# Optimization experiments

Hardware: AMD Instinct MI355X
Metric: run time of the kernel (lower is better)

## Reference

```python
import jax, jax.numpy as jnp
import numpy as np

B, L, E = 128, 512, 128
NUM_Q, NUM_C, DIFF = 10000, 300, 100


def _lin(k, fan_in, fan_out):
    kw, kb = jax.random.split(k)
    s = 1.0 / np.sqrt(fan_in)
    W = jax.random.uniform(kw, (fan_in, fan_out), jnp.float32, -s, s)
    b = jax.random.uniform(kb, (fan_out,), jnp.float32, -s, s)
    return W, b


def setup_inputs() -> dict:
    key = jax.random.key(0)
    ks = jax.random.split(key, 24)
    inp = {
        "q": jax.random.randint(ks[0], (B, L), 0, NUM_Q),
        "c": jax.random.randint(ks[1], (B, L), 0, NUM_C),
        "sd": jax.random.randint(ks[2], (B, L), 0, DIFF + 99),
        "qd": jax.random.randint(ks[3], (B, L), 0, DIFF + 99),
        "a": jax.random.randint(ks[4], (B, L), 0, 2 * NUM_Q + 1),
        "qshft": jax.random.randint(ks[5], (B, L), 0, NUM_Q),
        "cshft": jax.random.randint(ks[6], (B, L), 0, NUM_C),
        "sdshft": jax.random.randint(ks[7], (B, L), 0, DIFF + 99),
        "qdshft": jax.random.randint(ks[8], (B, L), 0, DIFF + 99),
        "knowledge": jax.random.normal(ks[9], (1, E), jnp.float32) * 0.1,
        "q_tab": jax.random.normal(ks[10], (NUM_Q + 1, E), jnp.float32),
        "c_tab": jax.random.normal(ks[11], (NUM_C + 1, E), jnp.float32),
        "sd_tab": jax.random.normal(ks[12], (DIFF + 100, E), jnp.float32),
        "qd_tab": jax.random.normal(ks[13], (DIFF + 100, E), jnp.float32),
        "a_tab": jax.random.normal(ks[14], (2 * NUM_Q + 2, E), jnp.float32),
    }
    for name, fan_in, ki in [("1", 4 * E, 15), ("2", E, 16), ("3", E, 17),
                             ("4", 2 * E, 18), ("5", 2 * E, 19), ("6", 4 * E, 20)]:
        W, b = _lin(ks[ki], fan_in, E)
        inp[f"W{name}"], inp[f"b{name}"] = W, b
    Wf, bf = _lin(ks[21], E, 10)
    inp["Wf"], inp["bf"] = Wf, bf
    return inp


def reference(q, c, sd, qd, a, qshft, cshft, sdshft, qdshft,
              knowledge, q_tab, c_tab, sd_tab, qd_tab, a_tab,
              W1, b1, W2, b2, W3, b3, W4, b4, W5, b5, W6, b6, Wf, bf):
    # Embedding lookups  [B, L, E]
    q_e, c_e = q_tab[q], c_tab[c]
    sd_e, qd_e = sd_tab[sd], qd_tab[qd]
    a_e = a_tab[a]
    # input_data = linear_1(cat(q,c,sd,qd))  [B, L, E]
    inp = jnp.concatenate([q_e, c_e, sd_e, qd_e], -1) @ W1 + b1
    # (target_data in the torch code is dead: never used for the output)

    k0 = jnp.broadcast_to(knowledge, (q.shape[0], knowledge.shape[1]))  # [B, E]

    def step(k, xs):
        x, sd1, a1, qd1 = xs  # each [B, E]
        qq = x - k
        SDFt = jax.nn.sigmoid(qq @ W2 + b2) * jnp.tanh(qq @ W3 + b3)  # dropout=eval
        xa = jnp.concatenate([SDFt, a1], -1)
        PKAt = jax.nn.sigmoid(xa @ W4 + b4) * jnp.tanh(xa @ W5 + b5)
        ins = jnp.concatenate([k, a1, sd1, qd1], -1)
        gK = jax.nn.sigmoid(ins @ W6 + b6)
        k_new = gK * k + (1.0 - gK) * PKAt
        return k_new, k_new @ Wf + bf

    xs = (jnp.swapaxes(inp, 0, 1), jnp.swapaxes(sd_e, 0, 1),
          jnp.swapaxes(a_e, 0, 1), jnp.swapaxes(qd_e, 0, 1))  # [L, B, E]
    _, logits = jax.lax.scan(step, k0, xs)  # [L, B, 10]
    return jax.nn.sigmoid(jnp.swapaxes(logits, 0, 1))  # [B, L, 10]
```

## Files before the change

kernel.cpp:

```cpp
#include <hip/hip_runtime.h>
#include <hip/hip_bf16.h>
#include <stdint.h>

#define E_DIM 128
#define L_SEQ 512
#define B_SZ  128

typedef _Float16 h2 __attribute__((ext_vector_type(2)));
typedef _Float16 f16x8 __attribute__((ext_vector_type(8)));
typedef float f32x4 __attribute__((ext_vector_type(4)));

constexpr size_t SZ_W12  = 512 * 128 * 4;
constexpr size_t SZ_TQ   = (size_t)10001 * 128 * 2 * 4;
constexpr size_t SZ_TC   = (size_t)301 * 128 * 2 * 4;
constexpr size_t SZ_TSD  = (size_t)200 * 128 * 4 * 4;
constexpr size_t SZ_TQD  = (size_t)200 * 128 * 4 * 4;
constexpr size_t SZ_TA45 = (size_t)20002 * 128 * 2 * 4;
constexpr size_t SZ_TA6  = (size_t)20002 * 128 * 4;
constexpr size_t SZ_K    = (size_t)B_SZ * L_SEQ * 128 * 4;

constexpr size_t OFF_W12  = 0;
constexpr size_t OFF_W13  = OFF_W12 + SZ_W12;
constexpr size_t OFF_BV2  = OFF_W13 + SZ_W12;
constexpr size_t OFF_BV3  = OFF_BV2 + 512;
constexpr size_t OFF_TQ   = OFF_BV3 + 512;
constexpr size_t OFF_TC   = OFF_TQ + SZ_TQ;
constexpr size_t OFF_TSD  = OFF_TC + SZ_TC;
constexpr size_t OFF_TQD  = OFF_TSD + SZ_TSD;
constexpr size_t OFF_TA45 = OFF_TQD + SZ_TQD;
constexpr size_t OFF_TA6  = OFF_TA45 + SZ_TA45;
constexpr size_t OFF_K    = OFF_TA6 + SZ_TA6;

__device__ __forceinline__ float fdot2f(unsigned int a, unsigned int b, float c) {
#if __has_builtin(__builtin_amdgcn_fdot2)
  return __builtin_amdgcn_fdot2(__builtin_bit_cast(h2, a), __builtin_bit_cast(h2, b), c, false);
#else
  h2 x = __builtin_bit_cast(h2, a), y = __builtin_bit_cast(h2, b);
  return c + (float)x[0] * (float)y[0] + (float)x[1] * (float)y[1];
#endif
}

__device__ __forceinline__ unsigned int packh2(float a, float b) {
  h2 v; v[0] = (_Float16)a; v[1] = (_Float16)b;
  return __builtin_bit_cast(unsigned int, v);
}

__device__ __forceinline__ float fsig(float x) {
  float t = __builtin_amdgcn_exp2f(-1.4426950408889634f * x);
  return __builtin_amdgcn_rcpf(1.0f + t);
}
__device__ __forceinline__ float ftanh(float x) {
  float t = __builtin_amdgcn_exp2f(2.8853900817779268f * x);
  return 1.0f - 2.0f * __builtin_amdgcn_rcpf(t + 1.0f);
}

#define BARRIER_RAW() asm volatile("s_waitcnt lgkmcnt(0)\n\ts_barrier" ::: "memory")

__global__ __launch_bounds__(256, 2) void prepA_kernel(
    const float* __restrict__ W1, const float* __restrict__ W2, const float* __restrict__ W3,
    const float* __restrict__ b1, const float* __restrict__ b2, const float* __restrict__ b3,
    char* __restrict__ ws) {
  float* W12 = (float*)(ws + OFF_W12);
  float* W13 = (float*)(ws + OFF_W13);
  float* bv2 = (float*)(ws + OFF_BV2);
  float* bv3 = (float*)(ws + OFF_BV3);
  const int blk = blockIdx.x, tid = threadIdx.x;
  if (blk < 512) {
    const int m = blk >> 8;
    const int rp = blk & 255;
    const float* M = m ? W3 : W2;
    float* dst = m ? W13 : W12;
    const int rr = tid >> 7, j = tid & 127;
    const int r = rp * 2 + rr;
    __shared__ float rowL[2][128];
    rowL[rr][j] = W1[r * 128 + j];
    __syncthreads();
    float acc = 0.0f;
#pragma unroll 8
    for (int t = 0; t < 128; t++) acc += rowL[rr][t] * M[t * 128 + j];
    dst[r * 128 + j] = acc;
  } else if (tid < 128) {
    float a2 = b2[tid], a3 = b3[tid];
    for (int t = 0; t < 128; t++) {
      float bb = b1[t];
      a2 += bb * W2[t * 128 + tid];
      a3 += bb * W3[t * 128 + tid];
    }
    bv2[tid] = a2;
    bv3[tid] = a3;
  }
}

__global__ __launch_bounds__(256, 2) void gemm_tab1_kernel(
    const float* __restrict__ q_tab, const float* __restrict__ c_tab,
    const float* __restrict__ sd_tab, const float* __restrict__ qd_tab,
    const float* __restrict__ a_tab,
    const float* __restrict__ W4, const float* __restrict__ W5, const float* __restrict__ W6,
    const float* __restrict__ b4, const float* __restrict__ b5, const float* __restrict__ b6,
    char* __restrict__ ws) {
  __shared__ _Float16 BT[128][136];
  __shared__ _Float16 At[32][136];
  __shared__ float biasL[128];

  const float* W12 = (const float*)(ws + OFF_W12);
  const float* W13 = (const float*)(ws + OFF_W13);
  const float* bv2f = (const float*)(ws + OFF_BV2);
  const float* bv3f = (const float*)(ws + OFF_BV3);

  const int bid = blockIdx.x, tid = threadIdx.x;
  const int wv = tid >> 6, ln = tid & 63;

  int task, rb;
  if      (bid < 79)  { task = 0;  rb = bid; }
  else if (bid < 158) { task = 1;  rb = bid - 79; }
  else if (bid < 161) { task = 2;  rb = bid - 158; }
  else if (bid < 164) { task = 3;  rb = bid - 161; }
  else if (bid < 166) { task = 4;  rb = bid - 164; }
  else if (bid < 168) { task = 5;  rb = bid - 166; }
  else if (bid < 170) { task = 6;  rb = bid - 168; }
  else if (bid < 172) { task = 7;  rb = bid - 170; }
  else if (bid < 174) { task = 8;  rb = bid - 172; }
  else if (bid < 176) { task = 9;  rb = bid - 174; }
  else if (bid < 333) { task = 10; rb = bid - 176; }
  else if (bid < 490) { task = 11; rb = bid - 333; }
  else                { task = 12; rb = bid - 490; }

  const float* src; int rows; const float* Bsrc; const float* bias;
  float* dst; int STR, ILV, SLOT;
  switch (task) {
    case 0:  src = q_tab;  rows = 10001; Bsrc = W12;           bias = bv2f;    dst = (float*)(ws + OFF_TQ);   STR = 256; ILV = 2; SLOT = 0; break;
    case 1:  src = q_tab;  rows = 10001; Bsrc = W13;           bias = bv3f;    dst = (float*)(ws + OFF_TQ);   STR = 256; ILV = 2; SLOT = 1; break;
    case 2:  src = c_tab;  rows = 301;   Bsrc = W12 + 128*128; bias = nullptr; dst = (float*)(ws + OFF_TC);   STR = 256; ILV = 2; SLOT = 0; break;
    case 3:  src = c_tab;  rows = 301;   Bsrc = W13 + 128*128; bias = nullptr; dst = (float*)(ws + OFF_TC);   STR = 256; ILV = 2; SLOT = 1; break;
    case 4:  src = sd_tab; rows = 200;   Bsrc = W12 + 256*128; bias = nullptr; dst = (float*)(ws + OFF_TSD);  STR = 512; ILV = 4; SLOT = 0; break;
    case 5:  src = sd_tab; rows = 200;   Bsrc = W13 + 256*128; bias = nullptr; dst = (float*)(ws + OFF_TSD);  STR = 512; ILV = 4; SLOT = 1; break;
    case 6:  src = sd_tab; rows = 200;   Bsrc = W6  + 256*128; bias = nullptr; dst = (float*)(ws + OFF_TSD);  STR = 512; ILV = 4; SLOT = 2; break;
    case 7:  src = qd_tab; rows = 200;   Bsrc = W12 + 384*128; bias = nullptr; dst = (float*)(ws + OFF_TQD);  STR = 512; ILV = 4; SLOT = 0; break;
    case 8:  src = qd_tab; rows = 200;   Bsrc = W13 + 384*128; bias = nullptr; dst = (float*)(ws + OFF_TQD);  STR = 512; ILV = 4; SLOT = 1; break;
    case 9:  src = qd_tab; rows = 200;   Bsrc = W6  + 384*128; bias = nullptr; dst = (float*)(ws + OFF_TQD);  STR = 512; ILV = 4; SLOT = 2; break;
    case 10: src = a_tab;  rows = 20002; Bsrc = W4  + 128*128; bias = b4;      dst = (float*)(ws + OFF_TA45); STR = 256; ILV = 2; SLOT = 0; break;
    case 11: src = a_tab;  rows = 20002; Bsrc = W5  + 128*128; bias = b5;      dst = (float*)(ws + OFF_TA45); STR = 256; ILV = 2; SLOT = 1; break;
    default: src = a_tab;  rows = 20002; Bsrc = W6  + 128*128; bias = b6;      dst = (float*)(ws + OFF_TA6);  STR = 128; ILV = 1; SLOT = 0; break;
  }

#pragma unroll
  for (int r = 0; r < 8; r++) {
    const int k = (tid >> 4) + r * 16;
    const int j0 = (tid & 15) * 8;
    float4 v0 = *(const float4*)(Bsrc + k * 128 + j0);
    float4 v1 = *(const float4*)(Bsrc + k * 128 + j0 + 4);
    BT[j0 + 0][k] = (_Float16)v0.x; BT[j0 + 1][k] = (_Float16)v0.y;
    BT[j0 + 2][k] = (_Float16)v0.z; BT[j0 + 3][k] = (_Float16)v0.w;
    BT[j0 + 4][k] = (_Float16)v1.x; BT[j0 + 5][k] = (_Float16)v1.y;
    BT[j0 + 6][k] = (_Float16)v1.z; BT[j0 + 7][k] = (_Float16)v1.w;
  }
  if (tid < 128) biasL[tid] = bias ? bias[tid] : 0.0f;
  __syncthreads();

  f16x8 bfr[2][4];
#pragma unroll
  for (int ct = 0; ct < 2; ct++)
#pragma unroll
    for (int kt = 0; kt < 4; kt++) {
      const int col = wv * 32 + ct * 16 + (ln & 15);
      const int k = kt * 32 + (ln >> 4) * 8;
      bfr[ct][kt] = *(const f16x8*)&BT[col][k];
    }
  float bvl[2] = { biasL[wv * 32 + (ln & 15)], biasL[wv * 32 + 16 + (ln & 15)] };

  const int row_base = rb * 128;
  for (int ch = 0; ch < 4; ch++) {
    const int row0 = row_base + ch * 32;
    {
      const int r = tid >> 3, cb = (tid & 7) * 16;
      int sr = row0 + r; if (sr >= rows) sr = rows - 1;
      const float4* s4 = (const float4*)(src + (size_t)sr * 128 + cb);
      float4 v0 = s4[0], v1 = s4[1], v2 = s4[2], v3 = s4[3];
      f16x8 lo, hi;
      lo[0] = (_Float16)v0.x; lo[1] = (_Float16)v0.y; lo[2] = (_Float16)v0.z; lo[3] = (_Float16)v0.w;
      lo[4] = (_Float16)v1.x; lo[5] = (_Float16)v1.y; lo[6] = (_Float16)v1.z; lo[7] = (_Float16)v1.w;
      hi[0] = (_Float16)v2.x; hi[1] = (_Float16)v2.y; hi[2] = (_Float16)v2.z; hi[3] = (_Float16)v2.w;
      hi[4] = (_Float16)v3.x; hi[5] = (_Float16)v3.y; hi[6] = (_Float16)v3.z; hi[7] = (_Float16)v3.w;
      *(f16x8*)&At[r][cb] = lo;
      *(f16x8*)&At[r][cb + 8] = hi;
    }
    __syncthreads();
    f16x8 af[2][4];
#pragma unroll
    for (int rt = 0; rt < 2; rt++)
#pragma unroll
      for (int kt = 0; kt < 4; kt++) {
        const int row = rt * 16 + (ln & 15);
        const int k = kt * 32 + (ln >> 4) * 8;
        af[rt][kt] = *(const f16x8*)&At[row][k];
      }
    f32x4 acc[2][2];
#pragma unroll
    for (int rt = 0; rt < 2; rt++)
#pragma unroll
      for (int ct = 0; ct < 2; ct++) acc[rt][ct] = (f32x4){0.f, 0.f, 0.f, 0.f};
#pragma unroll
    for (int kt = 0; kt < 4; kt++)
#pragma unroll
      for (int ct = 0; ct < 2; ct++)
#pragma unroll
        for (int rt = 0; rt < 2; rt++)
          acc[rt][ct] = __builtin_amdgcn_mfma_f32_16x16x32_f16(af[rt][kt], bfr[ct][kt], acc[rt][ct], 0, 0, 0);
#pragma unroll
    for (int ct = 0; ct < 2; ct++) {
      const int col = wv * 32 + ct * 16 + (ln & 15);
      const float bv = bvl[ct];
#pragma unroll
      for (int rt = 0; rt < 2; rt++)
#pragma unroll
        for (int e = 0; e < 4; e++) {
          const int row = row0 + rt * 16 + (ln >> 4) * 4 + e;
          if (row < rows) dst[(size_t)row * STR + col * ILV + SLOT] = acc[rt][ct][e] + bv;
        }
    }
    __syncthreads();
  }
}


#define PREFETCH(S, P) do {                                                   \
    int _s = (S);                                                             \
    int _qi = __builtin_amdgcn_readfirstlane(idxb[g][0][_s]);                 \
    int _ci = __builtin_amdgcn_readfirstlane(idxb[g][1][_s]);                 \
    int _si = __builtin_amdgcn_readfirstlane(idxb[g][2][_s]);                 \
    int _di = __builtin_amdgcn_readfirstlane(idxb[g][3][_s]);                 \
    int _ai = __builtin_amdgcn_readfirstlane(idxb[g][4][_s]);                 \
    P##q  = *(const float2*)(Tq   + ((size_t)_qi << 8) + (j << 1));           \
    P##c  = *(const float2*)(Tc   + ((size_t)_ci << 8) + (j << 1));           \
    P##s  = *(const float4*)(Ts   + ((size_t)_si << 9) + (j << 2));           \
    P##d  = *(const float4*)(Td   + ((size_t)_di << 9) + (j << 2));           \
    P##a  = *(const float2*)(Ta45 + ((size_t)_ai << 8) + (j << 1));           \
    P##a6 = Ta6[((size_t)_ai << 7) + j];                                      \
  } while (0)

#define SCAN_STEP(P, S2, L) do {                                              \
    float u2a = 0.f, u2b = 0.f, u3a = 0.f, u3b = 0.f, u6a = 0.f, u6b = 0.f;   \
    {                                                                         \
      const uint4* kp4 = ((const uint4*)kpair[g]) + 8 * h;                    \
      _Pragma("unroll")                                                       \
      for (int i = 0; i < 8; i++) {                                           \
        uint4 kv = kp4[i];                                                    \
        u2a = fdot2f(kv.x, w2h[4 * i + 0], u2a);                              \
        u3a = fdot2f(kv.x, w3h[4 * i + 0], u3a);                              \
        u6a = fdot2f(kv.x, w6h[4 * i + 0], u6a);                              \
        u2b = fdot2f(kv.y, w2h[4 * i + 1], u2b);                              \
        u3b = fdot2f(kv.y, w3h[4 * i + 1], u3b);                              \
        u6b = fdot2f(kv.y, w6h[4 * i + 1], u6b);                              \
        u2a = fdot2f(kv.z, w2h[4 * i + 2], u2a);                              \
        u3a = fdot2f(kv.z, w3h[4 * i + 2], u3a);                              \
        u6a = fdot2f(kv.z, w6h[4 * i + 2], u6a);                              \
        u2b = fdot2f(kv.w, w2h[4 * i + 3], u2b);                              \
        u3b = fdot2f(kv.w, w3h[4 * i + 3], u3b);                              \
        u6b = fdot2f(kv.w, w6h[4 * i + 3], u6b);                              \
      }                                                                       \
    }                                                                         \
    float U2p = u2a + u2b, U3p = u3a + u3b, U6p = u6a + u6b;                  \
    U2p += __shfl_xor(U2p, 32);                                               \
    U3p += __shfl_xor(U3p, 32);                                               \
    U6p += __shfl_xor(U6p, 32);                                               \
    float U2 = (P##q.x + P##c.x + P##s.x + P##d.x) - U2p;                     \
    float U3 = (P##q.y + P##c.y + P##s.y + P##d.y) - U3p;                     \
    float U6 = (P##a6 + P##s.z + P##d.z) + U6p;                               \
    float sdft = fsig(U2) * ftanh(U3);                                        \
    float g_ = fsig(U6);                                                      \
    if (!h) ((_Float16*)sdfp[g])[j] = (_Float16)sdft;                         \
    BARRIER_RAW();                                    \
    float u4a = 0.f, u4b = 0.f, u5a = 0.f, u5b = 0.f;                         \
    {                                                                         \
      const uint4* sp4 = ((const uint4*)sdfp[g]) + 8 * h;                     \
      _Pragma("unroll")                                                       \
      for (int i = 0; i < 8; i++) {                                           \
        uint4 sv = sp4[i];                                                    \
        u4a = fdot2f(sv.x, w4h[4 * i + 0], u4a);                              \
        u5a = fdot2f(sv.x, w5h[4 * i + 0], u5a);                              \
        u4b = fdot2f(sv.y, w4h[4 * i + 1], u4b);                              \
        u5b = fdot2f(sv.y, w5h[4 * i + 1], u5b);                              \
        u4a = fdot2f(sv.z, w4h[4 * i + 2], u4a);                              \
        u5a = fdot2f(sv.z, w5h[4 * i + 2], u5a);                              \
        u4b = fdot2f(sv.w, w4h[4 * i + 3], u4b);                              \
        u5b = fdot2f(sv.w, w5h[4 * i + 3], u5b);                              \
      }                                                                       \
    }                                                                         \
    float U4p = u4a + u4b, U5p = u5a + u5b;                                   \
    U4p += __shfl_xor(U4p, 32);                                               \
    U5p += __shfl_xor(U5p, 32);                                               \
    float pk = fsig(U4p + P##a.x) * ftanh(U5p + P##a.y);                      \
    k = g_ * k + (1.0f - g_) * pk;                                            \
    if (h) ((_Float16*)kpair[g])[j] = (_Float16)k;                            \
    if (!h) Kout[((size_t)(base + (L))) * 128 + j] = k;                       \
    PREFETCH(S2, P);                                                          \
    BARRIER_RAW();                                       \
  } while (0)

__global__ __launch_bounds__(512, 1) void scan_kernel(
    const int* __restrict__ q, const int* __restrict__ c, const int* __restrict__ sd,
    const int* __restrict__ qd, const int* __restrict__ a,
    const float* __restrict__ knowledge,
    const float* __restrict__ W2, const float* __restrict__ W3, const float* __restrict__ W4,
    const float* __restrict__ W5, const float* __restrict__ W6,
    char* __restrict__ ws) {
  const int tid = threadIdx.x;
  const int g = tid >> 8;
  const int t256 = tid & 255;
  const int ln = tid & 63;
  const int wvl = (t256 >> 6);
  const int j = (wvl << 5) | (ln & 31);
  const int h = ln >> 5;
  const int b = (blockIdx.x << 1) | g;
  const int base = b * L_SEQ;

  const float* Tq   = (const float*)(ws + OFF_TQ);
  const float* Tc   = (const float*)(ws + OFF_TC);
  const float* Ts   = (const float*)(ws + OFF_TSD);
  const float* Td   = (const float*)(ws + OFF_TQD);
  const float* Ta45 = (const float*)(ws + OFF_TA45);
  const float* Ta6  = (const float*)(ws + OFF_TA6);
  float* Kout = (float*)(ws + OFF_K);

  __shared__ int idxb[2][5][L_SEQ];
  __shared__ __align__(16) unsigned int kpair[2][64];
  __shared__ __align__(16) unsigned int sdfp[2][64];

  idxb[g][0][t256] = q[base + t256];  idxb[g][0][t256 + 256] = q[base + t256 + 256];
  idxb[g][1][t256] = c[base + t256];  idxb[g][1][t256 + 256] = c[base + t256 + 256];
  idxb[g][2][t256] = sd[base + t256]; idxb[g][2][t256 + 256] = sd[base + t256 + 256];
  idxb[g][3][t256] = qd[base + t256]; idxb[g][3][t256 + 256] = qd[base + t256 + 256];
  idxb[g][4][t256] = a[base + t256];  idxb[g][4][t256 + 256] = a[base + t256 + 256];

  unsigned int w2h[32], w3h[32], w6h[32], w4h[32], w5h[32];
  const int t0 = h * 64;
#pragma unroll
  for (int p = 0; p < 32; p++) {
    w2h[p] = packh2(W2[(t0 + 2 * p) * 128 + j], W2[(t0 + 2 * p + 1) * 128 + j]);
    w3h[p] = packh2(W3[(t0 + 2 * p) * 128 + j], W3[(t0 + 2 * p + 1) * 128 + j]);
    w6h[p] = packh2(W6[(t0 + 2 * p) * 128 + j], W6[(t0 + 2 * p + 1) * 128 + j]);
    w4h[p] = packh2(W4[(t0 + 2 * p) * 128 + j], W4[(t0 + 2 * p + 1) * 128 + j]);
    w5h[p] = packh2(W5[(t0 + 2 * p) * 128 + j], W5[(t0 + 2 * p + 1) * 128 + j]);
  }

  float k = knowledge[j];
  if (h) ((_Float16*)kpair[g])[j] = (_Float16)k;
  __syncthreads();

  float2 gAq, gAc, gAa; float4 gAs, gAd; float gAa6;
  float2 gBq, gBc, gBa; float4 gBs, gBd; float gBa6;
  PREFETCH(0, gA);
  PREFETCH(1, gB);

#pragma unroll 1
  for (int m = 0; m < L_SEQ / 2; m++) {
    const int l0 = 2 * m;
    const int s2 = (l0 + 2 < L_SEQ) ? (l0 + 2) : (L_SEQ - 1);
    const int s3 = (l0 + 3 < L_SEQ) ? (l0 + 3) : (L_SEQ - 1);
    SCAN_STEP(gA, s2, l0);
    SCAN_STEP(gB, s3, l0 + 1);
  }
}

__global__ __launch_bounds__(256, 2) void logits_kernel(
    const float* __restrict__ Wf, const float* __restrict__ bf,
    const char* __restrict__ ws, float* __restrict__ out) {
  __shared__ float WfL[1280];
  __shared__ float bfL[10];
  const int tid = threadIdx.x;
  for (int i = tid; i < 1280; i += 256) WfL[i] = Wf[i];
  if (tid < 10) bfL[tid] = bf[tid];
  __syncthreads();
  const float* K = (const float*)(ws + OFF_K);
  const int nrows = B_SZ * L_SEQ;
  for (int r = blockIdx.x * 256 + tid; r < nrows; r += gridDim.x * 256) {
    const float4* kr = (const float4*)(K + (size_t)r * 128);
    float acc[10];
#pragma unroll
    for (int i = 0; i < 10; i++) acc[i] = bfL[i];
#pragma unroll
    for (int t4 = 0; t4 < 32; t4++) {
      float4 v = kr[t4];
#pragma unroll
      for (int i = 0; i < 10; i++)
        acc[i] += v.x * WfL[(4 * t4 + 0) * 10 + i] + v.y * WfL[(4 * t4 + 1) * 10 + i] +
                  v.z * WfL[(4 * t4 + 2) * 10 + i] + v.w * WfL[(4 * t4 + 3) * 10 + i];
    }
    float* o = out + (size_t)r * 10;
#pragma unroll
    for (int i = 0; i < 10; i++) o[i] = fsig(acc[i]);
  }
}

extern "C" void kernel_launch(void* const* d_in, const int* in_sizes, int n_in,
                              void* d_out, int out_size, void* d_ws, size_t ws_size,
                              hipStream_t stream) {
  const int* q  = (const int*)d_in[0];
  const int* c  = (const int*)d_in[1];
  const int* sd = (const int*)d_in[2];
  const int* qd = (const int*)d_in[3];
  const int* a  = (const int*)d_in[4];
  const float* knowledge = (const float*)d_in[9];
  const float* q_tab  = (const float*)d_in[10];
  const float* c_tab  = (const float*)d_in[11];
  const float* sd_tab = (const float*)d_in[12];
  const float* qd_tab = (const float*)d_in[13];
  const float* a_tab  = (const float*)d_in[14];
  const float* W1 = (const float*)d_in[15];
  const float* b1 = (const float*)d_in[16];
  const float* W2 = (const float*)d_in[17];
  const float* b2 = (const float*)d_in[18];
  const float* W3 = (const float*)d_in[19];
  const float* b3 = (const float*)d_in[20];
  const float* W4 = (const float*)d_in[21];
  const float* b4 = (const float*)d_in[22];
  const float* W5 = (const float*)d_in[23];
  const float* b5 = (const float*)d_in[24];
  const float* W6 = (const float*)d_in[25];
  const float* b6 = (const float*)d_in[26];
  const float* Wf = (const float*)d_in[27];
  const float* bf = (const float*)d_in[28];
  char* ws = (char*)d_ws;
  float* out = (float*)d_out;

  prepA_kernel<<<513, 256, 0, stream>>>(W1, W2, W3, b1, b2, b3, ws);
  gemm_tab1_kernel<<<647, 256, 0, stream>>>(q_tab, c_tab, sd_tab, qd_tab, a_tab,
                                            W4, W5, W6, b4, b5, b6, ws);
  scan_kernel<<<B_SZ / 2, 512, 0, stream>>>(q, c, sd, qd, a, knowledge, W2, W3, W4, W5, W6, ws);
  logits_kernel<<<256, 256, 0, stream>>>(Wf, bf, ws, out);
}
```

Before: 888.2 us.

## Restructure scan to one 128-thread block per batch row with full-K per thread

The recurrent scan is restructured so each batch row gets its own 128-thread block, and each thread holds all 64 packed fp16 weight pairs for its output column. Previously two rows shared a 512-thread block, with each column split across two half-waves that needed a cross-lane shuffle reduction. The change removes the shuffles and half of the redundant stores, and spreads the work over 128 workgroups instead of 64. Weight packing moves into a small prep kernel, and the table GEMM stores are reindexed for a mode-based layout. In exchange, each thread now runs a serial dot-product chain twice as long and needs 320 weight registers, which raises register pressure and may cause spills.

Measured after the change: 1.338 ms. 1.51x slower.

```diff
diff --git a/kernel.cpp b/kernel.cpp
--- a/kernel.cpp
+++ b/kernel.cpp
@@ -18,6 +18,7 @@
 constexpr size_t SZ_TA45 = (size_t)20002 * 128 * 2 * 4;
 constexpr size_t SZ_TA6  = (size_t)20002 * 128 * 4;
 constexpr size_t SZ_K    = (size_t)B_SZ * L_SEQ * 128 * 4;
+constexpr size_t SZ_WP   = (size_t)5 * 64 * 128 * 4;
 
 constexpr size_t OFF_W12  = 0;
 constexpr size_t OFF_W13  = OFF_W12 + SZ_W12;
@@ -30,6 +31,7 @@
 constexpr size_t OFF_TA45 = OFF_TQD + SZ_TQD;
 constexpr size_t OFF_TA6  = OFF_TA45 + SZ_TA45;
 constexpr size_t OFF_K    = OFF_TA6 + SZ_TA6;
+constexpr size_t OFF_WP   = OFF_K + SZ_K;
 
 __device__ __forceinline__ float fdot2f(unsigned int a, unsigned int b, float c) {
 #if __has_builtin(__builtin_amdgcn_fdot2)
@@ -91,6 +93,19 @@
   }
 }
 
+__global__ __launch_bounds__(256, 2) void prepW_kernel(
+    const float* __restrict__ W2, const float* __restrict__ W3, const float* __restrict__ W4,
+    const float* __restrict__ W5, const float* __restrict__ W6, char* __restrict__ ws) {
+  unsigned int* WP = (unsigned int*)(ws + OFF_WP);
+  const float* src = (blockIdx.x == 0) ? W2 : (blockIdx.x == 1) ? W3 :
+                     (blockIdx.x == 2) ? W4 : (blockIdx.x == 3) ? W5 : W6;
+  unsigned int* dst = WP + (size_t)blockIdx.x * 8192;
+  for (int t = threadIdx.x; t < 8192; t += 256) {
+    const int p = t >> 7, jj = t & 127;
+    dst[t] = packh2(src[(2 * p) * 128 + jj], src[(2 * p + 1) * 128 + jj]);
+  }
+}
+
 __global__ __launch_bounds__(256, 2) void gemm_tab1_kernel(
     const float* __restrict__ q_tab, const float* __restrict__ c_tab,
     const float* __restrict__ sd_tab, const float* __restrict__ qd_tab,
@@ -126,21 +141,21 @@
   else                { task = 12; rb = bid - 490; }
 
   const float* src; int rows; const float* Bsrc; const float* bias;
-  float* dst; int STR, ILV, SLOT;
+  float* dst; int STR, MODE, SLOT;
   switch (task) {
-    case 0:  src = q_tab;  rows = 10001; Bsrc = W12;           bias = bv2f;    dst = (float*)(ws + OFF_TQ);   STR = 256; ILV = 2; SLOT = 0; break;
-    case 1:  src = q_tab;  rows = 10001; Bsrc = W13;           bias = bv3f;    dst = (float*)(ws + OFF_TQ);   STR = 256; ILV = 2; SLOT = 1; break;
-    case 2:  src = c_tab;  rows = 301;   Bsrc = W12 + 128*128; bias = nullptr; dst = (float*)(ws + OFF_TC);   STR = 256; ILV = 2; SLOT = 0; break;
-    case 3:  src = c_tab;  rows = 301;   Bsrc = W13 + 128*128; bias = nullptr; dst = (float*)(ws + OFF_TC);   STR = 256; ILV = 2; SLOT = 1; break;
-    case 4:  src = sd_tab; rows = 200;   Bsrc = W12 + 256*128; bias = nullptr; dst = (float*)(ws + OFF_TSD);  STR = 512; ILV = 4; SLOT = 0; break;
-    case 5:  src = sd_tab; rows = 200;   Bsrc = W13 + 256*128; bias = nullptr; dst = (float*)(ws + OFF_TSD);  STR = 512; ILV = 4; SLOT = 1; break;
-    case 6:  src = sd_tab; rows = 200;   Bsrc = W6  + 256*128; bias = nullptr; dst = (float*)(ws + OFF_TSD);  STR = 512; ILV = 4; SLOT = 2; break;
-    case 7:  src = qd_tab; rows = 200;   Bsrc = W12 + 384*128; bias = nullptr; dst = (float*)(ws + OFF_TQD);  STR = 512; ILV = 4; SLOT = 0; break;
-    case 8:  src = qd_tab; rows = 200;   Bsrc = W13 + 384*128; bias = nullptr; dst = (float*)(ws + OFF_TQD);  STR = 512; ILV = 4; SLOT = 1; break;
-    case 9:  src = qd_tab; rows = 200;   Bsrc = W6  + 384*128; bias = nullptr; dst = (float*)(ws + OFF_TQD);  STR = 512; ILV = 4; SLOT = 2; break;
-    case 10: src = a_tab;  rows = 20002; Bsrc = W4  + 128*128; bias = b4;      dst = (float*)(ws + OFF_TA45); STR = 256; ILV = 2; SLOT = 0; break;
-    case 11: src = a_tab;  rows = 20002; Bsrc = W5  + 128*128; bias = b5;      dst = (float*)(ws + OFF_TA45); STR = 256; ILV = 2; SLOT = 1; break;
-    default: src = a_tab;  rows = 20002; Bsrc = W6  + 128*128; bias = b6;      dst = (float*)(ws + OFF_TA6);  STR = 128; ILV = 1; SLOT = 0; break;
+    case 0:  src = q_tab;  rows = 10001; Bsrc = W12;           bias = bv2f;    dst = (float*)(ws + OFF_TQ);   STR = 256; MODE = 0; SLOT = 0; break;
+    case 1:  src = q_tab;  rows = 10001; Bsrc = W13;           bias = bv3f;    dst = (float*)(ws + OFF_TQ);   STR = 256; MODE = 0; SLOT = 1; break;
+    case 2:  src = c_tab;  rows = 301;   Bsrc = W12 + 128*128; bias = nullptr; dst = (float*)(ws + OFF_TC);   STR = 256; MODE = 0; SLOT = 0; break;
+    case 3:  src = c_tab;  rows = 301;   Bsrc = W13 + 128*128; bias = nullptr; dst = (float*)(ws + OFF_TC);   STR = 256; MODE = 0; SLOT = 1; break;
+    case 4:  src = sd_tab; rows = 200;   Bsrc = W12 + 256*128; bias = nullptr; dst = (float*)(ws + OFF_TSD);  STR = 512; MODE = 1; SLOT = 0; break;
+    case 5:  src = sd_tab; rows = 200;   Bsrc = W13 + 256*128; bias = nullptr; dst = (float*)(ws + OFF_TSD);  STR = 512; MODE = 1; SLOT = 1; break;
+    case 6:  src = sd_tab; rows = 200;   Bsrc = W6  + 256*128; bias = nullptr; dst = (float*)(ws + OFF_TSD);  STR = 512; MODE = 1; SLOT = 2; break;
+    case 7:  src = qd_tab; rows = 200;   Bsrc = W12 + 384*128; bias = nullptr; dst = (float*)(ws + OFF_TQD);  STR = 512; MODE = 1; SLOT = 0; break;
+    case 8:  src = qd_tab; rows = 200;   Bsrc = W13 + 384*128; bias = nullptr; dst = (float*)(ws + OFF_TQD);  STR = 512; MODE = 1; SLOT = 1; break;
+    case 9:  src = qd_tab; rows = 200;   Bsrc = W6  + 384*128; bias = nullptr; dst = (float*)(ws + OFF_TQD);  STR = 512; MODE = 1; SLOT = 2; break;
+    case 10: src = a_tab;  rows = 20002; Bsrc = W4  + 128*128; bias = b4;      dst = (float*)(ws + OFF_TA45); STR = 256; MODE = 0; SLOT = 0; break;
+    case 11: src = a_tab;  rows = 20002; Bsrc = W5  + 128*128; bias = b5;      dst = (float*)(ws + OFF_TA45); STR = 256; MODE = 0; SLOT = 1; break;
+    default: src = a_tab;  rows = 20002; Bsrc = W6  + 128*128; bias = b6;      dst = (float*)(ws + OFF_TA6);  STR = 128; MODE = 2; SLOT = 0; break;
   }
 
 #pragma unroll
@@ -209,13 +224,15 @@
 #pragma unroll
     for (int ct = 0; ct < 2; ct++) {
       const int col = wv * 32 + ct * 16 + (ln & 15);
+      const int cm = (MODE == 0) ? (((col >> 1) << 2) + ((col & 1) << 1) + SLOT)
+                   : (MODE == 1) ? ((col << 2) + SLOT) : col;
       const float bv = bvl[ct];
 #pragma unroll
       for (int rt = 0; rt < 2; rt++)
 #pragma unroll
         for (int e = 0; e < 4; e++) {
           const int row = row0 + rt * 16 + (ln >> 4) * 4 + e;
-          if (row < rows) dst[(size_t)row * STR + col * ILV + SLOT] = acc[rt][ct][e] + bv;
+          if (row < rows) dst[(size_t)row * STR + cm] = acc[rt][ct][e] + bv;
         }
     }
     __syncthreads();
@@ -225,11 +242,11 @@
 
 #define PREFETCH(S, P) do {                                                   \
     int _s = (S);                                                             \
-    int _qi = __builtin_amdgcn_readfirstlane(idxb[g][0][_s]);                 \
-    int _ci = __builtin_amdgcn_readfirstlane(idxb[g][1][_s]);                 \
-    int _si = __builtin_amdgcn_readfirstlane(idxb[g][2][_s]);                 \
-    int _di = __builtin_amdgcn_readfirstlane(idxb[g][3][_s]);                 \
-    int _ai = __builtin_amdgcn_readfirstlane(idxb[g][4][_s]);                 \
+    int _qi = __builtin_amdgcn_readfirstlane(idxb[0][_s]);                    \
+    int _ci = __builtin_amdgcn_readfirstlane(idxb[1][_s]);                    \
+    int _si = __builtin_amdgcn_readfirstlane(idxb[2][_s]);                    \
+    int _di = __builtin_amdgcn_readfirstlane(idxb[3][_s]);                    \
+    int _ai = __builtin_amdgcn_readfirstlane(idxb[4][_s]);                    \
     P##q  = *(const float2*)(Tq   + ((size_t)_qi << 8) + (j << 1));           \
     P##c  = *(const float2*)(Tc   + ((size_t)_ci << 8) + (j << 1));           \
     P##s  = *(const float4*)(Ts   + ((size_t)_si << 9) + (j << 2));           \
@@ -239,79 +256,66 @@
   } while (0)
 
 #define SCAN_STEP(P, S2, L) do {                                              \
+              \
     float u2a = 0.f, u2b = 0.f, u3a = 0.f, u3b = 0.f, u6a = 0.f, u6b = 0.f;   \
     {                                                                         \
-      const uint4* kp4 = ((const uint4*)kpair[g]) + 8 * h;                    \
+      const uint4* kp4 = (const uint4*)kpair;                                 \
       _Pragma("unroll")                                                       \
-      for (int i = 0; i < 8; i++) {                                           \
+      for (int i = 0; i < 16; i++) {                                          \
         uint4 kv = kp4[i];                                                    \
-        u2a = fdot2f(kv.x, w2h[4 * i + 0], u2a);                              \
-        u3a = fdot2f(kv.x, w3h[4 * i + 0], u3a);                              \
-        u6a = fdot2f(kv.x, w6h[4 * i + 0], u6a);                              \
-        u2b = fdot2f(kv.y, w2h[4 * i + 1], u2b);                              \
-        u3b = fdot2f(kv.y, w3h[4 * i + 1], u3b);                              \
-        u6b = fdot2f(kv.y, w6h[4 * i + 1], u6b);                              \
-        u2a = fdot2f(kv.z, w2h[4 * i + 2], u2a);                              \
-        u3a = fdot2f(kv.z, w3h[4 * i + 2], u3a);                              \
-        u6a = fdot2f(kv.z, w6h[4 * i + 2], u6a);                              \
-        u2b = fdot2f(kv.w, w2h[4 * i + 3], u2b);                              \
-        u3b = fdot2f(kv.w, w3h[4 * i + 3], u3b);                              \
-        u6b = fdot2f(kv.w, w6h[4 * i + 3], u6b);                              \
+        u2a = fdot2f(kv.x, w2[4 * i + 0], u2a);                               \
+        u3a = fdot2f(kv.x, w3[4 * i + 0], u3a);                               \
+        u6a = fdot2f(kv.x, w6[4 * i + 0], u6a);                               \
+        u2b = fdot2f(kv.y, w2[4 * i + 1], u2b);                               \
+        u3b = fdot2f(kv.y, w3[4 * i + 1], u3b);                               \
+        u6b = fdot2f(kv.y, w6[4 * i + 1], u6b);                               \
+        u2a = fdot2f(kv.z, w2[4 * i + 2], u2a);                               \
+        u3a = fdot2f(kv.z, w3[4 * i + 2], u3a);                               \
+        u6a = fdot2f(kv.z, w6[4 * i + 2], u6a);                               \
+        u2b = fdot2f(kv.w, w2[4 * i + 3], u2b);                               \
+        u3b = fdot2f(kv.w, w3[4 * i + 3], u3b);                               \
+        u6b = fdot2f(kv.w, w6[4 * i + 3], u6b);                               \
       }                                                                       \
     }                                                                         \
-    float U2p = u2a + u2b, U3p = u3a + u3b, U6p = u6a + u6b;                  \
-    U2p += __shfl_xor(U2p, 32);                                               \
-    U3p += __shfl_xor(U3p, 32);                                               \
-    U6p += __shfl_xor(U6p, 32);                                               \
-    float U2 = (P##q.x + P##c.x + P##s.x + P##d.x) - U2p;                     \
-    float U3 = (P##q.y + P##c.y + P##s.y + P##d.y) - U3p;                     \
-    float U6 = (P##a6 + P##s.z + P##d.z) + U6p;                               \
+    float U2 = (P##q.x + P##c.x + P##s.x + P##d.x) - (u2a + u2b);             \
+    float U3 = (P##q.y + P##c.y + P##s.y + P##d.y) - (u3a + u3b);             \
+    float U6 = (P##a6 + P##s.z + P##d.z) + (u6a + u6b);                       \
     float sdft = fsig(U2) * ftanh(U3);                                        \
     float g_ = fsig(U6);                                                      \
-    if (!h) ((_Float16*)sdfp[g])[j] = (_Float16)sdft;                         \
+    ((_Float16*)sdfp)[j] = (_Float16)sdft;                                    \
     BARRIER_RAW();                                    \
+                                   \
     float u4a = 0.f, u4b = 0.f, u5a = 0.f, u5b = 0.f;                         \
     {                                                                         \
-      const uint4* sp4 = ((const uint4*)sdfp[g]) + 8 * h;                     \
+      const uint4* sp4 = (const uint4*)sdfp;                                  \
       _Pragma("unroll")                                                       \
-      for (int i = 0; i < 8; i++) {                                           \
+      for (int i = 0; i < 16; i++) {                                          \
         uint4 sv = sp4[i];                                                    \
-        u4a = fdot2f(sv.x, w4h[4 * i + 0], u4a);                              \
-        u5a = fdot2f(sv.x, w5h[4 * i + 0], u5a);                              \
-        u4b = fdot2f(sv.y, w4h[4 * i + 1], u4b);                              \
-        u5b = fdot2f(sv.y, w5h[4 * i + 1], u5b);                              \
-        u4a = fdot2f(sv.z, w4h[4 * i + 2], u4a);                              \
-        u5a = fdot2f(sv.z, w5h[4 * i + 2], u5a);                              \
-        u4b = fdot2f(sv.w, w4h[4 * i + 3], u4b);                              \
-        u5b = fdot2f(sv.w, w5h[4 * i + 3], u5b);                              \
+        u4a = fdot2f(sv.x, w4[4 * i + 0], u4a);                               \
+        u5a = fdot2f(sv.x, w5[4 * i + 0], u5a);                               \
+        u4b = fdot2f(sv.y, w4[4 * i + 1], u4b);                               \
+        u5b = fdot2f(sv.y, w5[4 * i + 1], u5b);                               \
+        u4a = fdot2f(sv.z, w4[4 * i + 2], u4a);                               \
+        u5a = fdot2f(sv.z, w5[4 * i + 2], u5a);                               \
+        u4b = fdot2f(sv.w, w4[4 * i + 3], u4b);                               \
+        u5b = fdot2f(sv.w, w5[4 * i + 3], u5b);                               \
       }                                                                       \
     }                                                                         \
-    float U4p = u4a + u4b, U5p = u5a + u5b;                                   \
-    U4p += __shfl_xor(U4p, 32);                                               \
-    U5p += __shfl_xor(U5p, 32);                                               \
-    float pk = fsig(U4p + P##a.x) * ftanh(U5p + P##a.y);                      \
+    float pk = fsig(u4a + u4b + P##a.x) * ftanh(u5a + u5b + P##a.y);          \
     k = g_ * k + (1.0f - g_) * pk;                                            \
-    if (h) ((_Float16*)kpair[g])[j] = (_Float16)k;                            \
-    if (!h) Kout[((size_t)(base + (L))) * 128 + j] = k;                       \
+    ((_Float16*)kpair)[j] = (_Float16)k;                                      \
+    Kout[((size_t)(base + (L))) * 128 + j] = k;                               \
     PREFETCH(S2, P);                                                          \
     BARRIER_RAW();                                       \
   } while (0)
 
-__global__ __launch_bounds__(512, 1) void scan_kernel(
+__global__ __attribute__((amdgpu_flat_work_group_size(128, 128), amdgpu_waves_per_eu(1, 1)))
+void scan_kernel(
     const int* __restrict__ q, const int* __restrict__ c, const int* __restrict__ sd,
     const int* __restrict__ qd, const int* __restrict__ a,
-    const float* __restrict__ knowledge,
-    const float* __restrict__ W2, const float* __restrict__ W3, const float* __restrict__ W4,
-    const float* __restrict__ W5, const float* __restrict__ W6,
-    char* __restrict__ ws) {
-  const int tid = threadIdx.x;
-  const int g = tid >> 8;
-  const int t256 = tid & 255;
-  const int ln = tid & 63;
-  const int wvl = (t256 >> 6);
-  const int j = (wvl << 5) | (ln & 31);
-  const int h = ln >> 5;
-  const int b = (blockIdx.x << 1) | g;
+    const float* __restrict__ knowledge, char* __restrict__ ws) {
+  const int j = threadIdx.x;
+  const int b = blockIdx.x;
   const int base = b * L_SEQ;
 
   const float* Tq   = (const float*)(ws + OFF_TQ);
@@ -320,31 +324,32 @@
   const float* Td   = (const float*)(ws + OFF_TQD);
   const float* Ta45 = (const float*)(ws + OFF_TA45);
   const float* Ta6  = (const float*)(ws + OFF_TA6);
+  const unsigned int* WP = (const unsigned int*)(ws + OFF_WP);
   float* Kout = (float*)(ws + OFF_K);
 
-  __shared__ int idxb[2][5][L_SEQ];
-  __shared__ __align__(16) unsigned int kpair[2][64];
-  __shared__ __align__(16) unsigned int sdfp[2][64];
-
-  idxb[g][0][t256] = q[base + t256];  idxb[g][0][t256 + 256] = q[base + t256 + 256];
-  idxb[g][1][t256] = c[base + t256];  idxb[g][1][t256 + 256] = c[base + t256 + 256];
-  idxb[g][2][t256] = sd[base + t256]; idxb[g][2][t256 + 256] = sd[base + t256 + 256];
-  idxb[g][3][t256] = qd[base + t256]; idxb[g][3][t256 + 256] = qd[base + t256 + 256];
-  idxb[g][4][t256] = a[base + t256];  idxb[g][4][t256 + 256] = a[base + t256 + 256];
-
-  unsigned int w2h[32], w3h[32], w6h[32], w4h[32], w5h[32];
-  const int t0 = h * 64;
-#pragma unroll
-  for (int p = 0; p < 32; p++) {
-    w2h[p] = packh2(W2[(t0 + 2 * p) * 128 + j], W2[(t0 + 2 * p + 1) * 128 + j]);
-    w3h[p] = packh2(W3[(t0 + 2 * p) * 128 + j], W3[(t0 + 2 * p + 1) * 128 + j]);
-    w6h[p] = packh2(W6[(t0 + 2 * p) * 128 + j], W6[(t0 + 2 * p + 1) * 128 + j]);
-    w4h[p] = packh2(W4[(t0 + 2 * p) * 128 + j], W4[(t0 + 2 * p + 1) * 128 + j]);
-    w5h[p] = packh2(W5[(t0 + 2 * p) * 128 + j], W5[(t0 + 2 * p + 1) * 128 + j]);
+  __shared__ int idxb[5][L_SEQ];
+  __shared__ __align__(16) unsigned int kpair[64];
+  __shared__ __align__(16) unsigned int sdfp[64];
+
+#pragma unroll
+  for (int t = 0; t < 5; t++) {
+    const int* src = (t == 0) ? q : (t == 1) ? c : (t == 2) ? sd : (t == 3) ? qd : a;
+#pragma unroll
+    for (int r = 0; r < 4; r++) idxb[t][j + 128 * r] = src[base + j + 128 * r];
+  }
+
+  unsigned int w2[64], w3[64], w4[64], w5[64], w6[64];
+#pragma unroll
+  for (int p = 0; p < 64; p++) {
+    w2[p] = WP[p * 128 + j];
+    w3[p] = WP[8192 + p * 128 + j];
+    w4[p] = WP[2 * 8192 + p * 128 + j];
+    w5[p] = WP[3 * 8192 + p * 128 + j];
+    w6[p] = WP[4 * 8192 + p * 128 + j];
   }
 
   float k = knowledge[j];
-  if (h) ((_Float16*)kpair[g])[j] = (_Float16)k;
+  ((_Float16*)kpair)[j] = (_Float16)k;
   __syncthreads();
 
   float2 gAq, gAc, gAa; float4 gAs, gAd; float gAa6;
@@ -424,8 +429,9 @@
   float* out = (float*)d_out;
 
   prepA_kernel<<<513, 256, 0, stream>>>(W1, W2, W3, b1, b2, b3, ws);
+  prepW_kernel<<<5, 256, 0, stream>>>(W2, W3, W4, W5, W6, ws);
   gemm_tab1_kernel<<<647, 256, 0, stream>>>(q_tab, c_tab, sd_tab, qd_tab, a_tab,
                                             W4, W5, W6, b4, b5, b6, ws);
-  scan_kernel<<<B_SZ / 2, 512, 0, stream>>>(q, c, sd, qd, a, knowledge, W2, W3, W4, W5, W6, ws);
+  scan_kernel<<<B_SZ, 128, 0, stream>>>(q, c, sd, qd, a, knowledge, ws);
   logits_kernel<<<256, 256, 0, stream>>>(Wf, bf, ws, out);
 }
```
